# Optimization experiments

Measured on AMD Instinct MI355X. Metric: run time of the kernel, lower is better.

Reference implementation:

```python
import jax, jax.numpy as jnp
import numpy as np

S, D, DR = 131072, 512, 512

def setup_inputs() -> dict:
    key = jax.random.key(0)
    k1, k2, k3, k4, k5 = jax.random.split(key, 5)
    scale = 1.0 / np.sqrt(D)
    return {
        "att_vectors": jax.random.normal(k1, (S, D), dtype=jnp.float32),
        "ref_vector": jax.random.normal(k2, (1, DR), dtype=jnp.float32),
        "Wh": jax.random.normal(k3, (D, D), dtype=jnp.float32) * scale,
        "Wv": jax.random.normal(k4, (D, DR), dtype=jnp.float32) * scale,
        "Ws": jax.random.normal(k5, (1, D), dtype=jnp.float32) * scale,
    }

def reference(att_vectors, ref_vector, Wh, Wv, Ws):
    # h = tanh(att @ Wh^T + ref @ Wv^T)  -> [S, D] (ref broadcasts over S)
    h = jnp.tanh(att_vectors @ Wh.T + ref_vector @ Wv.T)
    # scores [S] -> softmax over sequence
    scores = (h @ Ws.T)[:, 0]
    w = jax.nn.softmax(scores)
    # fused weighted sum replacing the python loop: [D]
    return jnp.einsum("s,sd->d", w, att_vectors)
```

## Files before the change

kernel.cpp:

```cpp
#include <hip/hip_runtime.h>
#include <hip/hip_bf16.h>
#include <stdint.h>


#define D_DIM 512
#define BM 128

typedef __attribute__((ext_vector_type(8))) short short8;
typedef __attribute__((ext_vector_type(4))) float f32x4;

#define WS_BIAS 0
#define WS_OUT  512
#define WS_Z    1024
#define WS_MB   1025

__device__ __forceinline__ uint32_t bf16_1(float f) {
    uint32_t u = __float_as_uint(f);
    return (u + 0x7fffu + ((u >> 16) & 1u)) >> 16;
}
__device__ __forceinline__ uint32_t pack2(float a, float b) {
    return bf16_1(a) | (bf16_1(b) << 16);
}
__device__ __forceinline__ float bf2f(unsigned short b) {
    return __uint_as_float(((uint32_t)b) << 16);
}
__device__ __forceinline__ float fast_tanh(float x) {
    float a = fabsf(x);
    float e = __expf(2.0f * a);
    float t = 1.0f - 2.0f / (e + 1.0f);
    return copysignf(t, x);
}
template<int CTRL>
__device__ __forceinline__ float dpp_add(float v) {
    int i = __builtin_amdgcn_mov_dpp(__float_as_int(v), CTRL, 0xf, 0xf, true);
    return v + __int_as_float(i);
}
__device__ __forceinline__ float reduce16(float v) {
    v = dpp_add<0xB1>(v);
    v = dpp_add<0x4E>(v);
    v = dpp_add<0x141>(v);
    v = dpp_add<0x140>(v);
    return v;
}

__global__ void k0_prep(const float* __restrict__ ref, const float* __restrict__ Wv,
                        const float* __restrict__ Ws, float* __restrict__ wsb) {
    __shared__ float red[256];
    const int tid = threadIdx.x;
    const int w = tid >> 6, l = tid & 63;
    const int d = blockIdx.x * 4 + w;
    const f32x4* rp = (const f32x4*)ref;
    const f32x4* vp = (const f32x4*)(Wv + (size_t)d * D_DIM);
    f32x4 r0 = rp[2 * l], r1 = rp[2 * l + 1];
    f32x4 v0 = vp[2 * l], v1 = vp[2 * l + 1];
    float acc = r0[0]*v0[0] + r0[1]*v0[1] + r0[2]*v0[2] + r0[3]*v0[3]
              + r1[0]*v1[0] + r1[1]*v1[1] + r1[2]*v1[2] + r1[3]*v1[3];
    #pragma unroll
    for (int m = 1; m < 64; m <<= 1) acc += __shfl_xor(acc, m, 64);
    if (l == 0) wsb[WS_BIAS + d] = acc;

    if (blockIdx.x == 0) {
        wsb[WS_OUT + tid] = 0.0f;
        wsb[WS_OUT + 256 + tid] = 0.0f;
        if (tid == 0) wsb[WS_Z] = 0.0f;
        red[tid] = fabsf(Ws[tid]) + fabsf(Ws[tid + 256]);
        __syncthreads();
        for (int off = 128; off > 0; off >>= 1) {
            if (tid < off) red[tid] += red[tid + off];
            __syncthreads();
        }
        if (tid == 0) wsb[WS_MB] = red[0];
    }
}

__launch_bounds__(256, 2)
__global__ void k1_main(const float* __restrict__ att, const float* __restrict__ Wh,
                        const float* __restrict__ Ws, float* __restrict__ wsb) {
    __shared__ __align__(16) unsigned short Bt[2][4096];
    __shared__ float bias_s[512];
    __shared__ float wss_s[512];
    __shared__ float e_s[BM];
    __shared__ float out_s[512];

    const int tid = threadIdx.x;
    const int w   = tid >> 6;
    const int l   = tid & 63;
    const int l15 = l & 15;
    const int q   = l >> 4;
    const int row0 = blockIdx.x * BM;

    for (int i = tid; i < 512; i += 256) {
        bias_s[i] = wsb[WS_BIAS + i];
        wss_s[i]  = Ws[i];
        out_s[i]  = 0.0f;
    }
    const float mb = wsb[WS_MB];

    short8 afrag[2][16];
    #pragma unroll
    for (int t = 0; t < 2; ++t) {
        const int row = row0 + 32 * w + 16 * t + l15;
        const f32x4* ap = (const f32x4*)(att + (size_t)row * D_DIM + q * 8);
        #pragma unroll
        for (int kc = 0; kc < 16; ++kc) {
            f32x4 x0 = ap[kc * 8];
            f32x4 x1 = ap[kc * 8 + 1];
            union { short8 s; uint32_t u[4]; } af;
            af.u[0] = pack2(x0[0], x0[1]);
            af.u[1] = pack2(x0[2], x0[3]);
            af.u[2] = pack2(x1[0], x1[1]);
            af.u[3] = pack2(x1[2], x1[3]);
            afrag[t][kc] = af.s;
        }
    }

    f32x4 acc[2][8];
    #pragma unroll
    for (int t = 0; t < 2; ++t)
        #pragma unroll
        for (int n = 0; n < 8; ++n) acc[t][n] = (f32x4){0.f, 0.f, 0.f, 0.f};
    float sc[8] = {0.f, 0.f, 0.f, 0.f, 0.f, 0.f, 0.f, 0.f};

    const int c4   = tid & 7;
    const int nl0  = tid >> 3;
    const int kg   = c4 >> 1;
    const int joff = (c4 & 1) * 4;

    #pragma unroll
    for (int i = 0; i < 4; ++i) {
        const int n_loc = nl0 + 32 * i;
        const f32x4 v = *(const f32x4*)(Wh + (size_t)n_loc * D_DIM + c4 * 4);
        uint64_t p = (uint64_t)pack2(v[0], v[1]) | ((uint64_t)pack2(v[2], v[3]) << 32);
        *(uint64_t*)(&Bt[0][kg * 1024 + n_loc * 8 + joff]) = p;
    }

    for (int g = 0; g < 4; ++g) {
        #pragma unroll
        for (int kc = 0; kc < 16; ++kc) {
            const int buf = kc & 1;
            __syncthreads();
            f32x4 pre[4];
            const bool more = !(g == 3 && kc == 15);
            if (more) {
                const int gn  = (kc == 15) ? g + 1 : g;
                const int kcn = (kc + 1) & 15;
                #pragma unroll
                for (int i = 0; i < 4; ++i) {
                    const int n_loc = nl0 + 32 * i;
                    pre[i] = *(const f32x4*)(Wh + (size_t)(gn * 128 + n_loc) * D_DIM + kcn * 32 + c4 * 4);
                }
            }
            #pragma unroll
            for (int ns = 0; ns < 8; ++ns) {
                short8 bfr = *(const short8*)(&Bt[buf][(q * 128 + ns * 16 + l15) * 8]);
                acc[0][ns] = __builtin_amdgcn_mfma_f32_16x16x32_bf16(afrag[0][kc], bfr, acc[0][ns], 0, 0, 0);
                acc[1][ns] = __builtin_amdgcn_mfma_f32_16x16x32_bf16(afrag[1][kc], bfr, acc[1][ns], 0, 0, 0);
            }
            if (more) {
                const int bufn = buf ^ 1;
                #pragma unroll
                for (int i = 0; i < 4; ++i) {
                    const int n_loc = nl0 + 32 * i;
                    uint64_t p = (uint64_t)pack2(pre[i][0], pre[i][1]) | ((uint64_t)pack2(pre[i][2], pre[i][3]) << 32);
                    *(uint64_t*)(&Bt[bufn][kg * 1024 + n_loc * 8 + joff]) = p;
                }
            }
        }
        #pragma unroll
        for (int t = 0; t < 2; ++t) {
            #pragma unroll
            for (int ns = 0; ns < 8; ++ns) {
                const int c = g * 128 + ns * 16 + l15;
                const float bc = bias_s[c];
                const float wc = wss_s[c];
                f32x4 a = acc[t][ns];
                #pragma unroll
                for (int r = 0; r < 4; ++r)
                    sc[t * 4 + r] += fast_tanh(a[r] + bc) * wc;
                acc[t][ns] = (f32x4){0.f, 0.f, 0.f, 0.f};
            }
        }
    }

    #pragma unroll
    for (int i = 0; i < 8; ++i) sc[i] = reduce16(sc[i]);

    if (l15 == 0) {
        #pragma unroll
        for (int t = 0; t < 2; ++t)
            #pragma unroll
            for (int r = 0; r < 4; ++r)
                e_s[32 * w + 16 * t + q * 4 + r] = __expf(sc[t * 4 + r] - mb);
    }
    __syncthreads();

    if (w == 0) {
        float z = e_s[l] + e_s[l + 64];
        #pragma unroll
        for (int m = 1; m < 64; m <<= 1) z += __shfl_xor(z, m, 64);
        if (l == 0) atomicAdd(&wsb[WS_Z], z);
    }

    const float el0 = e_s[32 * w + l15];
    const float el1 = e_s[32 * w + 16 + l15];
    #pragma unroll
    for (int kc = 0; kc < 16; ++kc) {
        float o[8];
        #pragma unroll
        for (int j = 0; j < 8; ++j) {
            o[j] = el0 * bf2f((unsigned short)afrag[0][kc][j])
                 + el1 * bf2f((unsigned short)afrag[1][kc][j]);
            o[j] = reduce16(o[j]);
        }
        if (l15 == 0) {
            #pragma unroll
            for (int j = 0; j < 8; ++j)
                atomicAdd(&out_s[kc * 32 + q * 8 + j], o[j]);
        }
    }
    __syncthreads();
    for (int i = tid; i < 512; i += 256)
        atomicAdd(&wsb[WS_OUT + i], out_s[i]);
}

__global__ void k2_fin(const float* __restrict__ wsb, float* __restrict__ out) {
    const float z = wsb[WS_Z];
    out[threadIdx.x] = wsb[WS_OUT + threadIdx.x] / z;
}

extern "C" void kernel_launch(void* const* d_in, const int* in_sizes, int n_in,
                              void* d_out, int out_size, void* d_ws, size_t ws_size,
                              hipStream_t stream) {
    const float* att = (const float*)d_in[0];
    const float* ref = (const float*)d_in[1];
    const float* Wh  = (const float*)d_in[2];
    const float* Wv  = (const float*)d_in[3];
    const float* Ws  = (const float*)d_in[4];
    float* out = (float*)d_out;
    float* wsb = (float*)d_ws;

    hipLaunchKernelGGL(k0_prep, dim3(128), dim3(256), 0, stream, ref, Wv, Ws, wsb);
    hipLaunchKernelGGL(k1_main, dim3(131072 / BM), dim3(256), 0, stream, att, Wh, Ws, wsb);
    hipLaunchKernelGGL(k2_fin, dim3(1), dim3(512), 0, stream, wsb, out);
}
```

Baseline: 495.9 us.

## Pre-pack Wh to bf16 tiles and stream them into LDS with global_load_lds

A new kernel converts Wh to bf16 once per call, laid out in the MFMA B-fragment tile order, and stores it in the workspace. The main kernel then fills its double-buffered LDS tiles with direct global-to-LDS loads instead of loading fp32 Wh, converting it and writing to LDS in every block. This removes the per-block conversion work, register staging and half the weight bytes fetched, at the cost of an extra launch. The packed path is used only when the workspace is large enough, and pack2 now uses the HIP bf16 intrinsic.

```diff
diff --git a/kernel.cpp b/kernel.cpp
--- a/kernel.cpp
+++ b/kernel.cpp
@@ -13,13 +13,13 @@
 #define WS_OUT  512
 #define WS_Z    1024
 #define WS_MB   1025
-
-__device__ __forceinline__ uint32_t bf16_1(float f) {
-    uint32_t u = __float_as_uint(f);
-    return (u + 0x7fffu + ((u >> 16) & 1u)) >> 16;
-}
+#define BPK_FLOAT_OFF 2048
+#define WS_NEED_BYTES (8192 + 64 * 8192)
+
 __device__ __forceinline__ uint32_t pack2(float a, float b) {
-    return bf16_1(a) | (bf16_1(b) << 16);
+    union { __hip_bfloat162 h; uint32_t u; } cv;
+    cv.h = __float22bfloat162_rn(make_float2(a, b));
+    return cv.u;
 }
 __device__ __forceinline__ float bf2f(unsigned short b) {
     return __uint_as_float(((uint32_t)b) << 16);
@@ -41,6 +41,11 @@
     v = dpp_add<0x141>(v);
     v = dpp_add<0x140>(v);
     return v;
+}
+__device__ __forceinline__ void gl_lds16(const unsigned short* g, unsigned short* l) {
+    __builtin_amdgcn_global_load_lds(
+        (const __attribute__((address_space(1))) void*)g,
+        (__attribute__((address_space(3))) void*)l, 16, 0, 0);
 }
 
 __global__ void k0_prep(const float* __restrict__ ref, const float* __restrict__ Wv,
@@ -73,9 +78,31 @@
     }
 }
 
+__global__ void kB_pack(const float* __restrict__ Wh, unsigned short* __restrict__ bpk) {
+    const int t = blockIdx.x;
+    const int g = t >> 4, kc = t & 15;
+    #pragma unroll
+    for (int h = 0; h < 2; ++h) {
+        const int c = threadIdx.x + 256 * h;
+        const int q = c >> 7, ns = (c >> 4) & 7, l15 = c & 15;
+        const int n = g * 128 + ns * 16 + l15;
+        const int k0 = kc * 32 + q * 8;
+        const f32x4* wp = (const f32x4*)(Wh + (size_t)n * D_DIM + k0);
+        f32x4 x0 = wp[0], x1 = wp[1];
+        union { short8 s; uint32_t u[4]; } pk;
+        pk.u[0] = pack2(x0[0], x0[1]);
+        pk.u[1] = pack2(x0[2], x0[3]);
+        pk.u[2] = pack2(x1[0], x1[1]);
+        pk.u[3] = pack2(x1[2], x1[3]);
+        *(short8*)(bpk + (size_t)t * 4096 + (size_t)c * 8) = pk.s;
+    }
+}
+
+template<bool PRE>
 __launch_bounds__(256, 2)
 __global__ void k1_main(const float* __restrict__ att, const float* __restrict__ Wh,
-                        const float* __restrict__ Ws, float* __restrict__ wsb) {
+                        const float* __restrict__ Ws,
+                        const unsigned short* __restrict__ bpk, float* __restrict__ wsb) {
     __shared__ __align__(16) unsigned short Bt[2][4096];
     __shared__ float bias_s[512];
     __shared__ float wss_s[512];
@@ -88,6 +115,13 @@
     const int l15 = l & 15;
     const int q   = l >> 4;
     const int row0 = blockIdx.x * BM;
+
+    if constexpr (PRE) {
+        const unsigned short* s = bpk + (size_t)w * 1024 + (size_t)l * 8;
+        unsigned short* d = &Bt[0][w * 1024];
+        gl_lds16(s, d);
+        gl_lds16(s + 512, d + 512);
+    }
 
     for (int i = tid; i < 512; i += 256) {
         bias_s[i] = wsb[WS_BIAS + i];
@@ -126,12 +160,14 @@
     const int kg   = c4 >> 1;
     const int joff = (c4 & 1) * 4;
 
-    #pragma unroll
-    for (int i = 0; i < 4; ++i) {
-        const int n_loc = nl0 + 32 * i;
-        const f32x4 v = *(const f32x4*)(Wh + (size_t)n_loc * D_DIM + c4 * 4);
-        uint64_t p = (uint64_t)pack2(v[0], v[1]) | ((uint64_t)pack2(v[2], v[3]) << 32);
-        *(uint64_t*)(&Bt[0][kg * 1024 + n_loc * 8 + joff]) = p;
+    if constexpr (!PRE) {
+        #pragma unroll
+        for (int i = 0; i < 4; ++i) {
+            const int n_loc = nl0 + 32 * i;
+            const f32x4 v = *(const f32x4*)(Wh + (size_t)n_loc * D_DIM + c4 * 4);
+            uint64_t p = (uint64_t)pack2(v[0], v[1]) | ((uint64_t)pack2(v[2], v[3]) << 32);
+            *(uint64_t*)(&Bt[0][kg * 1024 + n_loc * 8 + joff]) = p;
+        }
     }
 
     for (int g = 0; g < 4; ++g) {
@@ -139,15 +175,25 @@
         for (int kc = 0; kc < 16; ++kc) {
             const int buf = kc & 1;
             __syncthreads();
+            const bool more = !(g == 3 && kc == 15);
             f32x4 pre[4];
-            const bool more = !(g == 3 && kc == 15);
-            if (more) {
-                const int gn  = (kc == 15) ? g + 1 : g;
-                const int kcn = (kc + 1) & 15;
-                #pragma unroll
-                for (int i = 0; i < 4; ++i) {
-                    const int n_loc = nl0 + 32 * i;
-                    pre[i] = *(const f32x4*)(Wh + (size_t)(gn * 128 + n_loc) * D_DIM + kcn * 32 + c4 * 4);
+            if constexpr (PRE) {
+                if (more) {
+                    const int tn = g * 16 + kc + 1;
+                    const unsigned short* s = bpk + (size_t)tn * 4096 + (size_t)w * 1024 + (size_t)l * 8;
+                    unsigned short* d = &Bt[buf ^ 1][w * 1024];
+                    gl_lds16(s, d);
+                    gl_lds16(s + 512, d + 512);
+                }
+            } else {
+                if (more) {
+                    const int gn  = (kc == 15) ? g + 1 : g;
+                    const int kcn = (kc + 1) & 15;
+                    #pragma unroll
+                    for (int i = 0; i < 4; ++i) {
+                        const int n_loc = nl0 + 32 * i;
+                        pre[i] = *(const f32x4*)(Wh + (size_t)(gn * 128 + n_loc) * D_DIM + kcn * 32 + c4 * 4);
+                    }
                 }
             }
             #pragma unroll
@@ -156,13 +202,15 @@
                 acc[0][ns] = __builtin_amdgcn_mfma_f32_16x16x32_bf16(afrag[0][kc], bfr, acc[0][ns], 0, 0, 0);
                 acc[1][ns] = __builtin_amdgcn_mfma_f32_16x16x32_bf16(afrag[1][kc], bfr, acc[1][ns], 0, 0, 0);
             }
-            if (more) {
-                const int bufn = buf ^ 1;
-                #pragma unroll
-                for (int i = 0; i < 4; ++i) {
-                    const int n_loc = nl0 + 32 * i;
-                    uint64_t p = (uint64_t)pack2(pre[i][0], pre[i][1]) | ((uint64_t)pack2(pre[i][2], pre[i][3]) << 32);
-                    *(uint64_t*)(&Bt[bufn][kg * 1024 + n_loc * 8 + joff]) = p;
+            if constexpr (!PRE) {
+                if (more) {
+                    const int bufn = buf ^ 1;
+                    #pragma unroll
+                    for (int i = 0; i < 4; ++i) {
+                        const int n_loc = nl0 + 32 * i;
+                        uint64_t p = (uint64_t)pack2(pre[i][0], pre[i][1]) | ((uint64_t)pack2(pre[i][2], pre[i][3]) << 32);
+                        *(uint64_t*)(&Bt[bufn][kg * 1024 + n_loc * 8 + joff]) = p;
+                    }
                 }
             }
         }
@@ -239,7 +287,17 @@
     float* out = (float*)d_out;
     float* wsb = (float*)d_ws;
 
+    unsigned short* bpk = (unsigned short*)(wsb + BPK_FLOAT_OFF);
+    const bool pre = ws_size >= (size_t)WS_NEED_BYTES;
+
     hipLaunchKernelGGL(k0_prep, dim3(128), dim3(256), 0, stream, ref, Wv, Ws, wsb);
-    hipLaunchKernelGGL(k1_main, dim3(131072 / BM), dim3(256), 0, stream, att, Wh, Ws, wsb);
+    if (pre) {
+        hipLaunchKernelGGL(kB_pack, dim3(64), dim3(256), 0, stream, Wh, bpk);
+        hipLaunchKernelGGL((k1_main<true>), dim3(131072 / BM), dim3(256), 0, stream,
+                           att, Wh, Ws, bpk, wsb);
+    } else {
+        hipLaunchKernelGGL((k1_main<false>), dim3(131072 / BM), dim3(256), 0, stream,
+                           att, Wh, Ws, bpk, wsb);
+    }
     hipLaunchKernelGGL(k2_fin, dim3(1), dim3(512), 0, stream, wsb, out);
 }
```

Result: faster. 479.1 us (-3.4%).

## Pre-pack Wh to bf16 MFMA layout and load B fragments directly from global

Applied to the files above, without the earlier changes.

Adds a small kernel that converts Wh to bf16 once, stored in the exact per-lane MFMA fragment order in workspace. The main kernel then reads B fragments straight from global/L2 instead of converting per block and double-buffering through LDS with a barrier every k-step. It also raises wave priority around the MFMA block and switches bf16 packing to the HIP intrinsic. This removes redundant per-block conversion work and LDS barriers, but relies on L2 bandwidth and latency for the B loads with no explicit prefetch.

```diff
diff --git a/kernel.cpp b/kernel.cpp
--- a/kernel.cpp
+++ b/kernel.cpp
@@ -13,13 +13,12 @@
 #define WS_OUT  512
 #define WS_Z    1024
 #define WS_MB   1025
-
-__device__ __forceinline__ uint32_t bf16_1(float f) {
-    uint32_t u = __float_as_uint(f);
-    return (u + 0x7fffu + ((u >> 16) & 1u)) >> 16;
-}
+#define BPK_FLOAT_OFF 2048
+
 __device__ __forceinline__ uint32_t pack2(float a, float b) {
-    return bf16_1(a) | (bf16_1(b) << 16);
+    union { __hip_bfloat162 h; uint32_t u; } cv;
+    cv.h = __float22bfloat162_rn(make_float2(a, b));
+    return cv.u;
 }
 __device__ __forceinline__ float bf2f(unsigned short b) {
     return __uint_as_float(((uint32_t)b) << 16);
@@ -73,10 +72,30 @@
     }
 }
 
+__global__ void kB_pack(const float* __restrict__ Wh, unsigned short* __restrict__ bpk) {
+    const int t = blockIdx.x;
+    const int g = t >> 4, kc = t & 15;
+    #pragma unroll
+    for (int h = 0; h < 2; ++h) {
+        const int c = threadIdx.x + 256 * h;
+        const int q = c >> 7, ns = (c >> 4) & 7, l15 = c & 15;
+        const int n = g * 128 + ns * 16 + l15;
+        const int k0 = kc * 32 + q * 8;
+        const f32x4* wp = (const f32x4*)(Wh + (size_t)n * D_DIM + k0);
+        f32x4 x0 = wp[0], x1 = wp[1];
+        union { short8 s; uint32_t u[4]; } pk;
+        pk.u[0] = pack2(x0[0], x0[1]);
+        pk.u[1] = pack2(x0[2], x0[3]);
+        pk.u[2] = pack2(x1[0], x1[1]);
+        pk.u[3] = pack2(x1[2], x1[3]);
+        *(short8*)(bpk + (size_t)t * 4096 + (size_t)c * 8) = pk.s;
+    }
+}
+
 __launch_bounds__(256, 2)
-__global__ void k1_main(const float* __restrict__ att, const float* __restrict__ Wh,
-                        const float* __restrict__ Ws, float* __restrict__ wsb) {
-    __shared__ __align__(16) unsigned short Bt[2][4096];
+__global__ void k1_main(const float* __restrict__ att,
+                        const float* __restrict__ Ws,
+                        const unsigned short* __restrict__ bpk, float* __restrict__ wsb) {
     __shared__ float bias_s[512];
     __shared__ float wss_s[512];
     __shared__ float e_s[BM];
@@ -121,50 +140,20 @@
         for (int n = 0; n < 8; ++n) acc[t][n] = (f32x4){0.f, 0.f, 0.f, 0.f};
     float sc[8] = {0.f, 0.f, 0.f, 0.f, 0.f, 0.f, 0.f, 0.f};
 
-    const int c4   = tid & 7;
-    const int nl0  = tid >> 3;
-    const int kg   = c4 >> 1;
-    const int joff = (c4 & 1) * 4;
-
-    #pragma unroll
-    for (int i = 0; i < 4; ++i) {
-        const int n_loc = nl0 + 32 * i;
-        const f32x4 v = *(const f32x4*)(Wh + (size_t)n_loc * D_DIM + c4 * 4);
-        uint64_t p = (uint64_t)pack2(v[0], v[1]) | ((uint64_t)pack2(v[2], v[3]) << 32);
-        *(uint64_t*)(&Bt[0][kg * 1024 + n_loc * 8 + joff]) = p;
-    }
+    const unsigned short* bl = bpk + (size_t)(q * 128 + l15) * 8;
 
     for (int g = 0; g < 4; ++g) {
         #pragma unroll
         for (int kc = 0; kc < 16; ++kc) {
-            const int buf = kc & 1;
-            __syncthreads();
-            f32x4 pre[4];
-            const bool more = !(g == 3 && kc == 15);
-            if (more) {
-                const int gn  = (kc == 15) ? g + 1 : g;
-                const int kcn = (kc + 1) & 15;
-                #pragma unroll
-                for (int i = 0; i < 4; ++i) {
-                    const int n_loc = nl0 + 32 * i;
-                    pre[i] = *(const f32x4*)(Wh + (size_t)(gn * 128 + n_loc) * D_DIM + kcn * 32 + c4 * 4);
-                }
-            }
+            const unsigned short* bt = bl + (size_t)(g * 16 + kc) * 4096;
+            __builtin_amdgcn_s_setprio(1);
             #pragma unroll
             for (int ns = 0; ns < 8; ++ns) {
-                short8 bfr = *(const short8*)(&Bt[buf][(q * 128 + ns * 16 + l15) * 8]);
+                short8 bfr = *(const short8*)(bt + ns * 128);
                 acc[0][ns] = __builtin_amdgcn_mfma_f32_16x16x32_bf16(afrag[0][kc], bfr, acc[0][ns], 0, 0, 0);
                 acc[1][ns] = __builtin_amdgcn_mfma_f32_16x16x32_bf16(afrag[1][kc], bfr, acc[1][ns], 0, 0, 0);
             }
-            if (more) {
-                const int bufn = buf ^ 1;
-                #pragma unroll
-                for (int i = 0; i < 4; ++i) {
-                    const int n_loc = nl0 + 32 * i;
-                    uint64_t p = (uint64_t)pack2(pre[i][0], pre[i][1]) | ((uint64_t)pack2(pre[i][2], pre[i][3]) << 32);
-                    *(uint64_t*)(&Bt[bufn][kg * 1024 + n_loc * 8 + joff]) = p;
-                }
-            }
+            __builtin_amdgcn_s_setprio(0);
         }
         #pragma unroll
         for (int t = 0; t < 2; ++t) {
@@ -239,7 +228,10 @@
     float* out = (float*)d_out;
     float* wsb = (float*)d_ws;
 
+    unsigned short* bpk = (unsigned short*)(wsb + BPK_FLOAT_OFF);
+
     hipLaunchKernelGGL(k0_prep, dim3(128), dim3(256), 0, stream, ref, Wv, Ws, wsb);
-    hipLaunchKernelGGL(k1_main, dim3(131072 / BM), dim3(256), 0, stream, att, Wh, Ws, wsb);
+    hipLaunchKernelGGL(kB_pack, dim3(64), dim3(256), 0, stream, Wh, bpk);
+    hipLaunchKernelGGL(k1_main, dim3(131072 / BM), dim3(256), 0, stream, att, Ws, bpk, wsb);
     hipLaunchKernelGGL(k2_fin, dim3(1), dim3(512), 0, stream, wsb, out);
 }
```

New measurement: 638.6 us. 28.8% more time.
